# Kernel tuning notes

Hardware: AMD Instinct MI355X
Metric: run time of the kernel (lower is better)

## Reference

```python
import jax, jax.numpy as jnp
import numpy as np

N = 8192
IN_F = 256
OUT_F = 128
E = 262144
NEG = -9e15


def setup_inputs() -> dict:
    key = jax.random.key(0)
    ks = jax.random.split(key, 12)
    glorot = lambda k, shp: jax.random.uniform(k, shp, jnp.float32,
                                               -jnp.sqrt(6.0 / (shp[0] + shp[1])),
                                               jnp.sqrt(6.0 / (shp[0] + shp[1])))
    return {
        "h_context": jax.random.normal(ks[0], (N, IN_F), jnp.float32),
        "h_structure": jax.random.normal(ks[1], (N, IN_F), jnp.float32),
        "edge_index": jax.random.randint(ks[2], (2, E), 0, N, jnp.int64),
        "Wc_w": glorot(ks[3], (OUT_F, IN_F)),
        "Wc_b": jnp.zeros((OUT_F,), jnp.float32),
        "Ws_w": glorot(ks[4], (OUT_F, IN_F)),
        "Ws_b": jnp.zeros((OUT_F,), jnp.float32),
        "ac_w": glorot(ks[5], (1, 2 * OUT_F)),
        "as_w": glorot(ks[6], (1, 2 * OUT_F)),
        "Ws_coff": jax.random.normal(ks[7], (1, 1), jnp.float32) * 1.414,
        "Wc_coff": jax.random.normal(ks[8], (1, 1), jnp.float32) * 1.414,
    }


def _pair_scores(h, a_w):
    # GAT trick: score[i,j] = leaky_relu(a1 . h[i] + a2 . h[j])
    F_out = h.shape[1]
    s_src = h @ a_w[0, :F_out]   # [N]
    s_dst = h @ a_w[0, F_out:]   # [N]
    return jax.nn.leaky_relu(s_src[:, None] + s_dst[None, :], 0.01)  # [N, N]


def reference(h_context, h_structure, edge_index, Wc_w, Wc_b, Ws_w, Ws_b,
              ac_w, as_w, Ws_coff, Wc_coff):
    hc = h_context @ Wc_w.T + Wc_b                      # [N, F]
    alpha_c = _pair_scores(hc, ac_w)                    # [N, N]
    hs = jax.nn.softmax(h_structure, axis=1) @ Ws_w.T + Ws_b
    alpha_s = _pair_scores(hs, as_w)                    # [N, N]
    alpha = jnp.abs(Ws_coff[0, 0]) * alpha_c + jnp.abs(Wc_coff[0, 0]) * alpha_s
    n = h_structure.shape[0]
    adj = jnp.zeros((n, n), bool).at[edge_index[0], edge_index[1]].set(True)
    attention = jnp.where(adj, alpha, NEG)
    attention = jax.nn.softmax(attention, axis=1)
    # dropout omitted (eval mode / deterministic reference)
    return attention @ hc
```

## Files before the change

### kernel.cpp

```cpp
#include <hip/hip_runtime.h>
#include <math.h>

#define N_NODES 8192
#define IN_FEAT 256
#define OUT_FEAT 128
#define CAP 128
#define M_TILE 32
#define NF_BLOCKS 512

typedef unsigned long long u64;
typedef float v4f __attribute__((ext_vector_type(4)));
typedef short s8v __attribute__((ext_vector_type(8)));
typedef short s4v __attribute__((ext_vector_type(4)));

__device__ __forceinline__ float wred_sum_b(float v) {
    #pragma unroll
    for (int o = 32; o > 0; o >>= 1) v += __shfl_xor(v, o, 64);
    return v;
}
__device__ __forceinline__ float wred_max_b(float v) {
    #pragma unroll
    for (int o = 32; o > 0; o >>= 1) v = fmaxf(v, __shfl_xor(v, o, 64));
    return v;
}

__device__ __forceinline__ void bsplit(float x, unsigned short& hi, unsigned short& lo) {
    unsigned int xb = __float_as_uint(x);
    hi = (unsigned short)(xb >> 16);
    float lof = x - __uint_as_float(xb & 0xFFFF0000u);
    lo = (unsigned short)(__float_as_uint(lof) >> 16);
}

__global__ __launch_bounds__(256) void prep(
    const float* __restrict__ Wc, const float* __restrict__ Ws,
    int* __restrict__ cnt,
    unsigned short* __restrict__ cfrag, unsigned short* __restrict__ sfrag)
{
    int tid = blockIdx.x * 256 + threadIdx.x;
    if (tid < 2048) ((int4*)cnt)[tid] = make_int4(0, 0, 0, 0);

    int mat = tid >> 13;
    int f = tid & 8191;
    int lnf = f & 63;
    int sel = (f >> 6) & 3;
    int ks  = (f >> 8) & 7;
    int wv  = (f >> 11) & 3;
    int row = (wv << 5) + ((sel >> 1) << 4) + (lnf & 15);
    int part = sel & 1;
    int k0 = (ks << 5) + ((lnf >> 4) << 3);
    const float* src = (mat ? Ws : Wc) + row * IN_FEAT + k0;
    short tmp[8];
    #pragma unroll
    for (int j = 0; j < 8; j++) {
        float x = src[j];
        unsigned int xb = __float_as_uint(x);
        if (part == 0) tmp[j] = (short)(xb >> 16);
        else {
            float lof = x - __uint_as_float(xb & 0xFFFF0000u);
            tmp[j] = (short)(__float_as_uint(lof) >> 16);
        }
    }
    unsigned short* dst = (mat ? sfrag : cfrag) + (size_t)f * 8;
    *(s8v*)dst = *(const s8v*)tmp;
}

__global__ __launch_bounds__(256, 4) void node_feats(
    const float* __restrict__ hctx, const float* __restrict__ hstr,
    const unsigned short* __restrict__ cfrag, const unsigned short* __restrict__ sfrag,
    const float* __restrict__ Wcb, const float* __restrict__ Wsb,
    const float* __restrict__ acw, const float* __restrict__ asw,
    const int* __restrict__ ei, int E,
    int* __restrict__ cnt, unsigned short* __restrict__ adj,
    float* __restrict__ hc,
    float* __restrict__ csrc, float* __restrict__ cdst,
    float* __restrict__ ssrc, float* __restrict__ sdst)
{
    __shared__ unsigned short aH[M_TILE][264], aL[M_TILE][264];
    __shared__ float invsh[M_TILE];
    float (*hT)[132] = (float(*)[132])&aH[0][0];

    const int t = threadIdx.x;
    const int w = t >> 6, ln = t & 63;
    const int is_struct = (blockIdx.x >= 256);
    const int b = blockIdx.x & 255;
    const int r0 = b * M_TILE;

    {
        int pv = ei[2 * (ln & 31) + 1];
        u64 nz = __ballot(pv != 0);
        const int is64 = (nz == 0);
        for (int e = blockIdx.x * 256 + t; e < E; e += NF_BLOCKS * 256) {
            int s, d;
            if (is64) { s = ei[2 * e]; d = ei[2 * E + 2 * e]; }
            else      { s = ei[e];     d = ei[E + e]; }
            if ((unsigned)s < N_NODES && (unsigned)d < N_NODES) {
                int idx = atomicAdd(&cnt[s], 1);
                if (idx < CAP) adj[(size_t)s * CAP + idx] = (unsigned short)d;
            }
        }
    }

    if (!is_struct) {
        #pragma unroll
        for (int j = 0; j < 8; j++) {
            int c = t + 256 * j;
            int r = c >> 6;
            int k = (c & 63) * 4;
            const float4 x = *(const float4*)(hctx + (size_t)(r0 + r) * IN_FEAT + k);
            unsigned short h0, h1, h2, h3, l0, l1, l2, l3;
            bsplit(x.x, h0, l0); bsplit(x.y, h1, l1);
            bsplit(x.z, h2, l2); bsplit(x.w, h3, l3);
            s4v hv = { (short)h0, (short)h1, (short)h2, (short)h3 };
            s4v lv = { (short)l0, (short)l1, (short)l2, (short)l3 };
            *(s4v*)&aH[r][k] = hv;
            *(s4v*)&aL[r][k] = lv;
        }
    } else {
        #pragma unroll
        for (int rr = 0; rr < 8; rr++) {
            int r = w * 8 + rr;
            const float* srow = hstr + (size_t)(r0 + r) * IN_FEAT;
            float x0 = srow[ln], x1 = srow[ln + 64], x2 = srow[ln + 128], x3 = srow[ln + 192];
            float mx = wred_max_b(fmaxf(fmaxf(x0, x1), fmaxf(x2, x3)));
            float e0 = __expf(x0 - mx), e1 = __expf(x1 - mx);
            float e2 = __expf(x2 - mx), e3 = __expf(x3 - mx);
            float s = wred_sum_b(e0 + e1 + e2 + e3);
            if (ln == 0) invsh[r] = 1.0f / s;
            unsigned short h, l;
            bsplit(e0, h, l); aH[r][ln]       = h; aL[r][ln]       = l;
            bsplit(e1, h, l); aH[r][ln + 64]  = h; aL[r][ln + 64]  = l;
            bsplit(e2, h, l); aH[r][ln + 128] = h; aL[r][ln + 128] = l;
            bsplit(e3, h, l); aH[r][ln + 192] = h; aL[r][ln + 192] = l;
        }
    }
    __syncthreads();

    const int m = ln & 15, q = ln >> 4;
    const unsigned short* frag = is_struct ? sfrag : cfrag;

    v4f a00 = {0.f,0.f,0.f,0.f}, a01 = {0.f,0.f,0.f,0.f};
    v4f a10 = {0.f,0.f,0.f,0.f}, a11 = {0.f,0.f,0.f,0.f};

    #pragma unroll 2
    for (int ks = 0; ks < 8; ks++) {
        const int k0 = ks * 32 + q * 8;
        const s8v* base = (const s8v*)frag + ((w * 8 + ks) * 4) * 64 + ln;
        s8v bh0 = base[0];
        s8v bl0 = base[64];
        s8v bh1 = base[128];
        s8v bl1 = base[192];
        s8v ah0 = *(const s8v*)&aH[m][k0];
        s8v al0 = *(const s8v*)&aL[m][k0];
        s8v ah1 = *(const s8v*)&aH[m + 16][k0];
        s8v al1 = *(const s8v*)&aL[m + 16][k0];
        a00 = __builtin_amdgcn_mfma_f32_16x16x32_bf16(al0, bh0, a00, 0, 0, 0);
        a00 = __builtin_amdgcn_mfma_f32_16x16x32_bf16(ah0, bl0, a00, 0, 0, 0);
        a00 = __builtin_amdgcn_mfma_f32_16x16x32_bf16(ah0, bh0, a00, 0, 0, 0);
        a01 = __builtin_amdgcn_mfma_f32_16x16x32_bf16(al0, bh1, a01, 0, 0, 0);
        a01 = __builtin_amdgcn_mfma_f32_16x16x32_bf16(ah0, bl1, a01, 0, 0, 0);
        a01 = __builtin_amdgcn_mfma_f32_16x16x32_bf16(ah0, bh1, a01, 0, 0, 0);
        a10 = __builtin_amdgcn_mfma_f32_16x16x32_bf16(al1, bh0, a10, 0, 0, 0);
        a10 = __builtin_amdgcn_mfma_f32_16x16x32_bf16(ah1, bl0, a10, 0, 0, 0);
        a10 = __builtin_amdgcn_mfma_f32_16x16x32_bf16(ah1, bh0, a10, 0, 0, 0);
        a11 = __builtin_amdgcn_mfma_f32_16x16x32_bf16(al1, bh1, a11, 0, 0, 0);
        a11 = __builtin_amdgcn_mfma_f32_16x16x32_bf16(ah1, bl1, a11, 0, 0, 0);
        a11 = __builtin_amdgcn_mfma_f32_16x16x32_bf16(ah1, bh1, a11, 0, 0, 0);
    }
    __syncthreads();

    const int nA = (w << 5) + m, nB = nA + 16;
    if (!is_struct) {
        const float bA = Wcb[nA], bB = Wcb[nB];
        #pragma unroll
        for (int p = 0; p < 4; p++) {
            int row = q * 4 + p;
            hT[row][nA]      = a00[p] + bA;
            hT[row][nB]      = a01[p] + bB;
            hT[row + 16][nA] = a10[p] + bA;
            hT[row + 16][nB] = a11[p] + bB;
        }
        __syncthreads();

        #pragma unroll
        for (int j = 0; j < 16; j++) {
            int f = t + 256 * j;
            int r = f >> 7, c = f & 127;
            hc[(size_t)(r0 + r) * OUT_FEAT + c] = hT[r][c];
        }
        float a0 = acw[ln], a0b = acw[ln + 64], a1 = acw[128 + ln], a1b = acw[192 + ln];
        #pragma unroll
        for (int rr = 0; rr < 8; rr++) {
            int r = w * 8 + rr;
            float c0 = hT[r][ln], c1 = hT[r][ln + 64];
            float v0 = wred_sum_b(c0 * a0 + c1 * a0b);
            float v1 = wred_sum_b(c0 * a1 + c1 * a1b);
            if (ln == 0) { csrc[r0 + r] = v0; cdst[r0 + r] = v1; }
        }
    } else {
        const float bA = Wsb[nA], bB = Wsb[nB];
        float iv0[4], iv1[4];
        #pragma unroll
        for (int p = 0; p < 4; p++) { iv0[p] = invsh[q * 4 + p]; iv1[p] = invsh[q * 4 + p + 16]; }
        #pragma unroll
        for (int p = 0; p < 4; p++) {
            int row = q * 4 + p;
            hT[row][nA]      = a00[p] * iv0[p] + bA;
            hT[row][nB]      = a01[p] * iv0[p] + bB;
            hT[row + 16][nA] = a10[p] * iv1[p] + bA;
            hT[row + 16][nB] = a11[p] * iv1[p] + bB;
        }
        __syncthreads();

        float b0 = asw[ln], b0b = asw[ln + 64], b1 = asw[128 + ln], b1b = asw[192 + ln];
        #pragma unroll
        for (int rr = 0; rr < 8; rr++) {
            int r = w * 8 + rr;
            float s0 = hT[r][ln], s1 = hT[r][ln + 64];
            float v2 = wred_sum_b(s0 * b0 + s1 * b0b);
            float v3 = wred_sum_b(s0 * b1 + s1 * b1b);
            if (ln == 0) { ssrc[r0 + r] = v2; sdst[r0 + r] = v3; }
        }
    }
}

__global__ __launch_bounds__(256) void attn(
    const int* __restrict__ cntArr, const unsigned short* __restrict__ adj,
    const float* __restrict__ hc,
    const float* __restrict__ csrc, const float* __restrict__ cdst,
    const float* __restrict__ ssrc, const float* __restrict__ sdst,
    const float* __restrict__ wscoff, const float* __restrict__ wccoff,
    float* __restrict__ out)
{
    __shared__ int   jl[4][CAP];
    __shared__ float pl[4][CAP];

    const int w  = threadIdx.x >> 6;
    const int ln = threadIdx.x & 63;
    const int i  = blockIdx.x * 4 + w;

    const float wS = fabsf(wscoff[0]);
    const float wC = fabsf(wccoff[0]);
    const float cs = csrc[i], ss = ssrc[i];

    int cnt = cntArr[i];
    if (cnt > CAP) cnt = CAP;

    if (cnt == 0) {
        float2 acc = {0.f, 0.f};
        const float2* hc2f = (const float2*)hc;
        for (int j = 0; j < N_NODES; j++) {
            float2 h2 = hc2f[(size_t)j * 64 + ln];
            acc.x += h2.x; acc.y += h2.y;
        }
        float2 o2 = { acc.x / (float)N_NODES, acc.y / (float)N_NODES };
        *(float2*)(out + (size_t)i * OUT_FEAT + 2 * ln) = o2;
        return;
    }

    const unsigned short* row = adj + (size_t)i * CAP;
    int j0 = (ln < cnt)      ? (int)row[ln]      : -1;
    int j1 = (64 + ln < cnt) ? (int)row[64 + ln] : -1;
    jl[w][ln] = j0;
    jl[w][64 + ln] = j1;
    __threadfence_block();

    bool dup0 = false, dup1 = false;
    if (j0 >= 0) {
        for (int k2 = 0; k2 < ln; k2++) dup0 |= (jl[w][k2] == j0);
    }
    if (__ballot(j1 >= 0)) {
        if (j1 >= 0) {
            for (int k2 = 0; k2 < 64 + ln; k2++) dup1 |= (jl[w][k2] == j1);
        }
    }

    float al0 = -3e38f, al1 = -3e38f;
    if (j0 >= 0 && !dup0) {
        float ac  = cs + cdst[j0];
        float as_ = ss + sdst[j0];
        ac  = (ac  > 0.0f) ? ac  : 0.01f * ac;
        as_ = (as_ > 0.0f) ? as_ : 0.01f * as_;
        al0 = wS * ac + wC * as_;
    }
    if (j1 >= 0 && !dup1) {
        float ac  = cs + cdst[j1];
        float as_ = ss + sdst[j1];
        ac  = (ac  > 0.0f) ? ac  : 0.01f * ac;
        as_ = (as_ > 0.0f) ? as_ : 0.01f * as_;
        al1 = wS * ac + wC * as_;
    }

    float m = wred_max_b(fmaxf(al0, al1));
    float p0 = __expf(al0 - m);
    float p1 = __expf(al1 - m);
    float s = wred_sum_b(p0 + p1);
    float inv = 1.0f / s;

    pl[w][ln] = p0;
    pl[w][64 + ln] = p1;
    __threadfence_block();

    const float2* hc2 = (const float2*)hc;
    float2 acc = {0.f, 0.f};
    int k = 0;
    for (; k + 8 <= cnt; k += 8) {
        float2 hx[8];
        float  px[8];
        #pragma unroll
        for (int u = 0; u < 8; u++) {
            int ju = jl[w][k + u];
            px[u] = pl[w][k + u];
            hx[u] = hc2[(size_t)ju * 64 + ln];
        }
        #pragma unroll
        for (int u = 0; u < 8; u++) {
            acc.x += px[u] * hx[u].x;
            acc.y += px[u] * hx[u].y;
        }
    }
    for (; k < cnt; k++) {
        float2 h0 = hc2[(size_t)jl[w][k] * 64 + ln];
        float pp = pl[w][k];
        acc.x += pp * h0.x; acc.y += pp * h0.y;
    }
    float2 o2 = { acc.x * inv, acc.y * inv };
    *(float2*)(out + (size_t)i * OUT_FEAT + 2 * ln) = o2;
}

extern "C" void kernel_launch(void* const* d_in, const int* in_sizes, int n_in,
                              void* d_out, int out_size, void* d_ws, size_t ws_size,
                              hipStream_t stream)
{
    const float* hctx = (const float*)d_in[0];
    const float* hstr = (const float*)d_in[1];
    const int*   ei   = (const int*)d_in[2];
    const float* Wc   = (const float*)d_in[3];
    const float* Wcb  = (const float*)d_in[4];
    const float* Ws   = (const float*)d_in[5];
    const float* Wsb  = (const float*)d_in[6];
    const float* acw  = (const float*)d_in[7];
    const float* asw  = (const float*)d_in[8];
    const float* wsco = (const float*)d_in[9];
    const float* wcco = (const float*)d_in[10];
    float* out = (float*)d_out;

    const int n2 = in_sizes[2];
    const int E  = (n2 == 4 * 262144) ? 262144 : n2 / 2;

    char* ws = (char*)d_ws;
    size_t off = 0;
    float* hc   = (float*)(ws + off); off += (size_t)N_NODES * OUT_FEAT * sizeof(float);
    float* csrc = (float*)(ws + off); off += (size_t)N_NODES * sizeof(float);
    float* cdst = (float*)(ws + off); off += (size_t)N_NODES * sizeof(float);
    float* ssrc = (float*)(ws + off); off += (size_t)N_NODES * sizeof(float);
    float* sdst = (float*)(ws + off); off += (size_t)N_NODES * sizeof(float);
    off = (off + 255) & ~(size_t)255;
    int* cnt = (int*)(ws + off);      off += (size_t)N_NODES * sizeof(int);
    unsigned short* adj = (unsigned short*)(ws + off); off += (size_t)N_NODES * CAP * sizeof(unsigned short);
    unsigned short* cfrag = (unsigned short*)(ws + off); off += (size_t)8192 * 8 * sizeof(unsigned short);
    unsigned short* sfrag = (unsigned short*)(ws + off); off += (size_t)8192 * 8 * sizeof(unsigned short);

    prep<<<64, 256, 0, stream>>>(Wc, Ws, cnt, cfrag, sfrag);
    node_feats<<<NF_BLOCKS, 256, 0, stream>>>(hctx, hstr, cfrag, sfrag, Wcb, Wsb,
                                              acw, asw, ei, E, cnt, adj,
                                              hc, csrc, cdst, ssrc, sdst);
    attn<<<N_NODES / 4, 256, 0, stream>>>(cnt, adj, hc, csrc, cdst, ssrc, sdst,
                                          wsco, wcco, out);
}
```

Baseline: 119.8 us.

## Vectorize edge loads, use LDS bitmap dedup, float4 half-wave gather in attention

```diff
diff --git a/kernel.cpp b/kernel.cpp
--- a/kernel.cpp
+++ b/kernel.cpp
@@ -88,14 +88,26 @@
     {
         int pv = ei[2 * (ln & 31) + 1];
         u64 nz = __ballot(pv != 0);
-        const int is64 = (nz == 0);
-        for (int e = blockIdx.x * 256 + t; e < E; e += NF_BLOCKS * 256) {
-            int s, d;
-            if (is64) { s = ei[2 * e]; d = ei[2 * E + 2 * e]; }
-            else      { s = ei[e];     d = ei[E + e]; }
-            if ((unsigned)s < N_NODES && (unsigned)d < N_NODES) {
-                int idx = atomicAdd(&cnt[s], 1);
-                if (idx < CAP) adj[(size_t)s * CAP + idx] = (unsigned short)d;
+        if (nz == 0) {
+            for (int e2 = (blockIdx.x * 256 + t) * 2; e2 < E; e2 += NF_BLOCKS * 512) {
+                int4 sv = *(const int4*)(ei + 2 * e2);
+                int4 dv = *(const int4*)(ei + 2 * E + 2 * e2);
+                if ((unsigned)sv.x < N_NODES && (unsigned)dv.x < N_NODES) {
+                    int idx = atomicAdd(&cnt[sv.x], 1);
+                    if (idx < CAP) adj[(size_t)sv.x * CAP + idx] = (unsigned short)dv.x;
+                }
+                if (e2 + 1 < E && (unsigned)sv.z < N_NODES && (unsigned)dv.z < N_NODES) {
+                    int idx = atomicAdd(&cnt[sv.z], 1);
+                    if (idx < CAP) adj[(size_t)sv.z * CAP + idx] = (unsigned short)dv.z;
+                }
+            }
+        } else {
+            for (int e = blockIdx.x * 256 + t; e < E; e += NF_BLOCKS * 256) {
+                int s = ei[e], d = ei[E + e];
+                if ((unsigned)s < N_NODES && (unsigned)d < N_NODES) {
+                    int idx = atomicAdd(&cnt[s], 1);
+                    if (idx < CAP) adj[(size_t)s * CAP + idx] = (unsigned short)d;
+                }
             }
         }
     }
@@ -231,8 +243,9 @@
     const float* __restrict__ wscoff, const float* __restrict__ wccoff,
     float* __restrict__ out)
 {
-    __shared__ int   jl[4][CAP];
-    __shared__ float pl[4][CAP];
+    __shared__ int          jl[4][CAP];
+    __shared__ float        pl[4][CAP];
+    __shared__ unsigned int bm[4][256];
 
     const int w  = threadIdx.x >> 6;
     const int ln = threadIdx.x & 63;
@@ -257,6 +270,11 @@
         return;
     }
 
+    bm[w][ln]       = 0u;
+    bm[w][ln + 64]  = 0u;
+    bm[w][ln + 128] = 0u;
+    bm[w][ln + 192] = 0u;
+
     const unsigned short* row = adj + (size_t)i * CAP;
     int j0 = (ln < cnt)      ? (int)row[ln]      : -1;
     int j1 = (64 + ln < cnt) ? (int)row[64 + ln] : -1;
@@ -264,25 +282,25 @@
     jl[w][64 + ln] = j1;
     __threadfence_block();
 
-    bool dup0 = false, dup1 = false;
+    bool keep0 = false, keep1 = false;
     if (j0 >= 0) {
-        for (int k2 = 0; k2 < ln; k2++) dup0 |= (jl[w][k2] == j0);
-    }
-    if (__ballot(j1 >= 0)) {
-        if (j1 >= 0) {
-            for (int k2 = 0; k2 < 64 + ln; k2++) dup1 |= (jl[w][k2] == j1);
-        }
+        unsigned int bit = 1u << (j0 & 31);
+        keep0 = !(atomicOr(&bm[w][j0 >> 5], bit) & bit);
+    }
+    if (j1 >= 0) {
+        unsigned int bit = 1u << (j1 & 31);
+        keep1 = !(atomicOr(&bm[w][j1 >> 5], bit) & bit);
     }
 
     float al0 = -3e38f, al1 = -3e38f;
-    if (j0 >= 0 && !dup0) {
+    if (keep0) {
         float ac  = cs + cdst[j0];
         float as_ = ss + sdst[j0];
         ac  = (ac  > 0.0f) ? ac  : 0.01f * ac;
         as_ = (as_ > 0.0f) ? as_ : 0.01f * as_;
         al0 = wS * ac + wC * as_;
     }
-    if (j1 >= 0 && !dup1) {
+    if (keep1) {
         float ac  = cs + cdst[j1];
         float as_ = ss + sdst[j1];
         ac  = (ac  > 0.0f) ? ac  : 0.01f * ac;
@@ -300,31 +318,46 @@
     pl[w][64 + ln] = p1;
     __threadfence_block();
 
-    const float2* hc2 = (const float2*)hc;
-    float2 acc = {0.f, 0.f};
+    const int half = ln >> 5;
+    const int c4   = ln & 31;
+    const float4* hc4 = (const float4*)hc;
+    float4 acc = {0.f, 0.f, 0.f, 0.f};
+
     int k = 0;
     for (; k + 8 <= cnt; k += 8) {
-        float2 hx[8];
-        float  px[8];
-        #pragma unroll
-        for (int u = 0; u < 8; u++) {
-            int ju = jl[w][k + u];
-            px[u] = pl[w][k + u];
-            hx[u] = hc2[(size_t)ju * 64 + ln];
-        }
-        #pragma unroll
-        for (int u = 0; u < 8; u++) {
+        float4 hx[4];
+        float  px[4];
+        #pragma unroll
+        for (int u = 0; u < 4; u++) {
+            int idx = k + 2 * u + half;
+            px[u] = pl[w][idx];
+            hx[u] = hc4[(size_t)jl[w][idx] * 32 + c4];
+        }
+        #pragma unroll
+        for (int u = 0; u < 4; u++) {
             acc.x += px[u] * hx[u].x;
             acc.y += px[u] * hx[u].y;
-        }
-    }
-    for (; k < cnt; k++) {
-        float2 h0 = hc2[(size_t)jl[w][k] * 64 + ln];
-        float pp = pl[w][k];
-        acc.x += pp * h0.x; acc.y += pp * h0.y;
-    }
-    float2 o2 = { acc.x * inv, acc.y * inv };
-    *(float2*)(out + (size_t)i * OUT_FEAT + 2 * ln) = o2;
+            acc.z += px[u] * hx[u].z;
+            acc.w += px[u] * hx[u].w;
+        }
+    }
+    for (; k < cnt; k += 2) {
+        int idx = k + half;
+        float p = (idx < cnt) ? pl[w][idx] : 0.0f;
+        int j = jl[w][(idx < cnt) ? idx : 0];
+        float4 h = hc4[(size_t)j * 32 + c4];
+        acc.x += p * h.x; acc.y += p * h.y;
+        acc.z += p * h.z; acc.w += p * h.w;
+    }
+
+    acc.x += __shfl_xor(acc.x, 32, 64);
+    acc.y += __shfl_xor(acc.y, 32, 64);
+    acc.z += __shfl_xor(acc.z, 32, 64);
+    acc.w += __shfl_xor(acc.w, 32, 64);
+    if (half == 0) {
+        float4 o4 = { acc.x * inv, acc.y * inv, acc.z * inv, acc.w * inv };
+        *(float4*)(out + (size_t)i * OUT_FEAT + 4 * c4) = o4;
+    }
 }
 
 extern "C" void kernel_launch(void* const* d_in, const int* in_sizes, int n_in,
```

New measurement: 117.6 us. No clear change (-1.8%).
